# Optimization experiments

Hardware: AMD Instinct MI355X
Metric: run time of the kernel (lower is better)

## Reference

```python
import jax, jax.numpy as jnp
import numpy as np

B, T1, T2, F, H = 4, 1024, 2048, 1024, 16
DK = F // H


def setup_inputs() -> dict:
    key = jax.random.key(0)
    ks = jax.random.split(key, 9)
    s = 1.0 / np.sqrt(F)
    return {
        "x": jax.random.normal(ks[0], (B, T1, F), dtype=jnp.float32),
        "memory": jax.random.normal(ks[1], (B, T2, F), dtype=jnp.float32),
        "memory_mask": jax.random.randint(ks[2], (B, 1, T2), 0, 2, dtype=jnp.int32),
        "Wq": jax.random.normal(ks[3], (F, F), dtype=jnp.float32) * s,
        "bq": jnp.zeros((F,), dtype=jnp.float32),
        "Wkv": jax.random.normal(ks[4], (F, 2 * F), dtype=jnp.float32) * s,
        "bkv": jnp.zeros((2 * F,), dtype=jnp.float32),
        "Wo": jax.random.normal(ks[5], (F, F), dtype=jnp.float32) * s,
        "bo": jnp.zeros((F,), dtype=jnp.float32),
    }


def reference(x, memory, memory_mask, Wq, bq, Wkv, bkv, Wo, bo):
    b = x.shape[0]
    # QKV projections
    q = (x @ Wq + bq).reshape(b, -1, H, DK).transpose(0, 2, 1, 3)      # [b,h,t1,dk]
    kv = memory @ Wkv + bkv
    k, v = jnp.split(kv, 2, axis=-1)
    k = k.reshape(b, -1, H, DK).transpose(0, 2, 1, 3)                   # [b,h,t2,dk]
    v = v.reshape(b, -1, H, DK).transpose(0, 2, 1, 3)                   # [b,h,t2,dk]
    # scaled dot-product scores [b,h,t1,t2]
    scores = jnp.einsum("bhqd,bhkd->bhqk", q * (DK ** -0.5), k)
    # mask (b,1,t2) -> (b,1,1,t2); eq(0) means masked out
    m = (memory_mask[:, None, :, :] == 0)
    scores = jnp.where(m, -jnp.inf, scores)
    attn = jax.nn.softmax(scores, axis=-1)
    attn = jnp.where(m, 0.0, attn)
    out = jnp.einsum("bhqk,bhkd->bhqd", attn, v)                        # [b,h,t1,dk]
    out = out.transpose(0, 2, 1, 3).reshape(b, -1, H * DK)              # [b,t1,F]
    return out @ Wo + bo
```

## Files before the change

kernel.cpp:

```cpp
#include <hip/hip_runtime.h>

typedef unsigned short u16;
typedef __attribute__((ext_vector_type(8))) short bf16x8;
typedef __attribute__((ext_vector_type(4))) float f32x4;
typedef __attribute__((ext_vector_type(4))) unsigned u32x4;

#define DEVI __device__ __forceinline__

static constexpr int B_ = 4, T1 = 1024, T2 = 2048, F = 1024, H = 16, DK = 64;

typedef __attribute__((address_space(3))) unsigned lds_u32;
typedef __attribute__((address_space(1))) const unsigned gmem_u32;

DEVI u16 f2bf(float f) {
    union { float f; unsigned u; } c; c.f = f;
    unsigned u = c.u + 0x7fffu + ((c.u >> 16) & 1u);
    return (u16)(u >> 16);
}

__global__ __launch_bounds__(256) void cast2_bf16_k(const float* __restrict__ a, u16* __restrict__ da, int na,
                                                    const float* __restrict__ b, u16* __restrict__ db, int ntot) {
    int i = (blockIdx.x * 256 + threadIdx.x) * 4;
    if (i >= ntot) return;
    const float* s = (i < na) ? a : b;
    u16* d = (i < na) ? da : db;
    int off = (i < na) ? i : i - na;
    float4 v = *(const float4*)(s + off);
    ushort4 o;
    o.x = f2bf(v.x); o.y = f2bf(v.y); o.z = f2bf(v.z); o.w = f2bf(v.w);
    *(ushort4*)(d + off) = o;
}

__global__ __launch_bounds__(256) void transpose_cast_k(const float* __restrict__ src0,
                                                        u16* __restrict__ dst0,
                                                        const float* __restrict__ src1,
                                                        u16* __restrict__ dst1,
                                                        int K, int N) {
    const float* src = blockIdx.z ? src1 : src0;
    u16* dst = blockIdx.z ? dst1 : dst0;
    __shared__ float tile[64][65];
    int kb = blockIdx.x * 64, nb = blockIdx.y * 64;
    int tx = threadIdx.x & 63, ty = threadIdx.x >> 6;
#pragma unroll
    for (int p = 0; p < 16; ++p) {
        int r = p * 4 + ty;
        tile[r][tx] = src[(size_t)(kb + r) * N + nb + tx];
    }
    __syncthreads();
#pragma unroll
    for (int p = 0; p < 16; ++p) {
        int r = p * 4 + ty;
        dst[(size_t)(nb + r) * K + kb + tx] = f2bf(tile[tx][r]);
    }
}

template <bool OUT_BF16, int WM, int WN>
__global__ __launch_bounds__(256) void gemm_k(const u16* __restrict__ A,
                                              const u16* __restrict__ Bt,
                                              const float* __restrict__ bias,
                                              float scale,
                                              void* __restrict__ Cout,
                                              int M, int N, int K) {
    constexpr int BM = 2 * WM, BN = 2 * WN;
    __shared__ u16 ldsA[2][BM * 64];
    __shared__ u16 ldsB[2][BN * 64];
    const int t = threadIdx.x;
    const int w = t >> 6, lane = t & 63;
    const int wr = w >> 1, wc = w & 1;
    const int lr = lane & 15, lg = lane >> 4;

    const int r0 = t >> 3;
    const int cl = (t & 7) ^ (r0 & 7);
    const u16* Ag = A + (size_t)(blockIdx.x * BM + r0) * K + cl * 8;
    const u16* Bg = Bt + (size_t)(blockIdx.y * BN + r0) * K + cl * 8;

#define GSTAGE(BUF, KOFF) \
    { \
        _Pragma("unroll") \
        for (int i_ = 0; i_ < BM / 32; ++i_) \
            __builtin_amdgcn_global_load_lds( \
                (gmem_u32*)(Ag + (size_t)i_ * 32 * K + (KOFF)), \
                (lds_u32*)((char*)&ldsA[BUF][0] + i_ * 4096 + w * 1024), 16, 0, 0); \
        _Pragma("unroll") \
        for (int i_ = 0; i_ < BN / 32; ++i_) \
            __builtin_amdgcn_global_load_lds( \
                (gmem_u32*)(Bg + (size_t)i_ * 32 * K + (KOFF)), \
                (lds_u32*)((char*)&ldsB[BUF][0] + i_ * 4096 + w * 1024), 16, 0, 0); \
    }

    f32x4 acc[WM / 16][WN / 16] = {};

    GSTAGE(0, 0);
    __syncthreads();

    int buf = 0;
    for (int k0 = 0; k0 < K; k0 += 64) {
        if (k0 + 64 < K) GSTAGE(buf ^ 1, k0 + 64);

        bf16x8 a[2][WM / 16], b[2][WN / 16];
#pragma unroll
        for (int kk = 0; kk < 2; ++kk) {
#pragma unroll
            for (int m = 0; m < WM / 16; ++m) {
                int ra = wr * WM + m * 16 + lr;
                a[kk][m] = *(const bf16x8*)&ldsA[buf][ra * 64 + (((kk * 4 + lg) ^ (ra & 7)) * 8)];
            }
#pragma unroll
            for (int n = 0; n < WN / 16; ++n) {
                int rb = wc * WN + n * 16 + lr;
                b[kk][n] = *(const bf16x8*)&ldsB[buf][rb * 64 + (((kk * 4 + lg) ^ (rb & 7)) * 8)];
            }
        }
#pragma unroll
        for (int kk = 0; kk < 2; ++kk)
#pragma unroll
            for (int m = 0; m < WM / 16; ++m)
#pragma unroll
                for (int n = 0; n < WN / 16; ++n)
                    acc[m][n] = __builtin_amdgcn_mfma_f32_16x16x32_bf16(a[kk][m], b[kk][n], acc[m][n], 0, 0, 0);
        __syncthreads();
        buf ^= 1;
    }

    const int rbase = blockIdx.x * BM + wr * WM;
    const int cbase = blockIdx.y * BN + wc * WN;
#pragma unroll
    for (int m = 0; m < WM / 16; ++m)
#pragma unroll
        for (int n = 0; n < WN / 16; ++n) {
            int col = cbase + n * 16 + lr;
            float bv = bias ? bias[col] : 0.f;
#pragma unroll
            for (int j = 0; j < 4; ++j) {
                int row = rbase + m * 16 + lg * 4 + j;
                float v = (acc[m][n][j] + bv) * scale;
                if (OUT_BF16)
                    ((u16*)Cout)[(size_t)row * N + col] = f2bf(v);
                else
                    ((float*)Cout)[(size_t)row * N + col] = v;
            }
        }
#undef GSTAGE
}

__global__ __launch_bounds__(256) void gemm_kv_k(const u16* __restrict__ A,
                                                 const u16* __restrict__ Bt,
                                                 const float* __restrict__ bias,
                                                 u16* __restrict__ Kb,
                                                 u16* __restrict__ Vt) {
    constexpr int K = F, N = F;
    __shared__ u16 smem[4][128 * 64];
    const int t = threadIdx.x;
    const int w = t >> 6, lane = t & 63;
    const int wr = w >> 1, wc = w & 1;
    const int lr = lane & 15, lg = lane >> 4;

    const int r0 = t >> 3;
    const int cl = (t & 7) ^ (r0 & 7);
    const u16* Ag = A + (size_t)(blockIdx.x * 128 + r0) * K + cl * 8;
    const u16* Bg = Bt + (size_t)(blockIdx.y * 128 + r0) * K + cl * 8;

#define KVSTAGE(BUF, KOFF) \
    { \
        _Pragma("unroll") \
        for (int i_ = 0; i_ < 4; ++i_) { \
            __builtin_amdgcn_global_load_lds( \
                (gmem_u32*)(Ag + (size_t)i_ * 32 * K + (KOFF)), \
                (lds_u32*)((char*)&smem[BUF][0] + i_ * 4096 + w * 1024), 16, 0, 0); \
            __builtin_amdgcn_global_load_lds( \
                (gmem_u32*)(Bg + (size_t)i_ * 32 * K + (KOFF)), \
                (lds_u32*)((char*)&smem[2 + (BUF)][0] + i_ * 4096 + w * 1024), 16, 0, 0); \
        } \
    }

    f32x4 acc[4][4] = {};

    KVSTAGE(0, 0);
    __syncthreads();

    int buf = 0;
    for (int k0 = 0; k0 < K; k0 += 64) {
        if (k0 + 64 < K) KVSTAGE(buf ^ 1, k0 + 64);

        bf16x8 a[2][4], b[2][4];
#pragma unroll
        for (int kk = 0; kk < 2; ++kk)
#pragma unroll
            for (int m = 0; m < 4; ++m) {
                int ra = wr * 64 + m * 16 + lr;
                int rb = wc * 64 + m * 16 + lr;
                a[kk][m] = *(const bf16x8*)&smem[buf][ra * 64 + (((kk * 4 + lg) ^ (ra & 7)) * 8)];
                b[kk][m] = *(const bf16x8*)&smem[2 + buf][rb * 64 + (((kk * 4 + lg) ^ (rb & 7)) * 8)];
            }
#pragma unroll
        for (int kk = 0; kk < 2; ++kk)
#pragma unroll
            for (int m = 0; m < 4; ++m)
#pragma unroll
                for (int n = 0; n < 4; ++n)
                    acc[m][n] = __builtin_amdgcn_mfma_f32_16x16x32_bf16(a[kk][m], b[kk][n], acc[m][n], 0, 0, 0);
        __syncthreads();
        buf ^= 1;
    }

    const int rbase = blockIdx.x * 128 + wr * 64;
    if (blockIdx.y < 8) {
        const int cbase = blockIdx.y * 128 + wc * 64;
#pragma unroll
        for (int m = 0; m < 4; ++m)
#pragma unroll
            for (int n = 0; n < 4; ++n) {
                int col = cbase + n * 16 + lr;
                float bv = bias[col];
#pragma unroll
                for (int j = 0; j < 4; ++j) {
                    int row = rbase + m * 16 + lg * 4 + j;
                    Kb[(size_t)row * N + col] = f2bf(acc[m][n][j] + bv);
                }
            }
    } else {
        u16* tbuf = &smem[0][0];
        const int cb2 = (blockIdx.y - 8) * 128;
#pragma unroll
        for (int m = 0; m < 4; ++m)
#pragma unroll
            for (int n = 0; n < 4; ++n) {
                int c = wc * 64 + n * 16 + lr;
                float bv = bias[F + cb2 + c];
#pragma unroll
                for (int j = 0; j < 4; ++j) {
                    int r = wr * 64 + m * 16 + lg * 4 + j;
                    int np = ((r >> 2) & 3) * 16 + ((r >> 5) & 1) * 8 + ((r >> 4) & 1) * 4 + (r & 3) + (r & 64);
                    tbuf[c * 136 + np] = f2bf(acc[m][n][j] + bv);
                }
            }
        __syncthreads();
        const int c = t >> 1, half = t & 1;
        const int rb = blockIdx.x * 128;
        const int b = rb >> 11, t2b = rb & 2047;
        const int vcol = cb2 + c;
        const int hh = vcol >> 6, d = vcol & 63;
        u16* dst = Vt + ((size_t)((b * H + hh) * DK + d)) * T2 + t2b + half * 64;
        const u16* srcp = &tbuf[c * 136 + half * 64];
#pragma unroll
        for (int i = 0; i < 8; ++i)
            *(uint4*)(dst + i * 8) = *(const uint4*)(srcp + i * 8);
    }
#undef KVSTAGE
}

#define SOFTMAX_PACK(S, PA0, PA1) \
    { \
        float pv_[4][4]; \
        _Pragma("unroll") \
        for (int ss_ = 0; ss_ < 4; ++ss_) \
            _Pragma("unroll") \
            for (int j_ = 0; j_ < 4; ++j_) \
                pv_[ss_][j_] = __builtin_amdgcn_exp2f(S[ss_][j_]); \
        u32x4 pw0_, pw1_; \
        asm("v_cvt_pk_bf16_f32 %0, %1, %2" : "=v"(pw0_[0]) : "v"(pv_[0][0]), "v"(pv_[0][1])); \
        asm("v_cvt_pk_bf16_f32 %0, %1, %2" : "=v"(pw0_[1]) : "v"(pv_[0][2]), "v"(pv_[0][3])); \
        asm("v_cvt_pk_bf16_f32 %0, %1, %2" : "=v"(pw0_[2]) : "v"(pv_[1][0]), "v"(pv_[1][1])); \
        asm("v_cvt_pk_bf16_f32 %0, %1, %2" : "=v"(pw0_[3]) : "v"(pv_[1][2]), "v"(pv_[1][3])); \
        asm("v_cvt_pk_bf16_f32 %0, %1, %2" : "=v"(pw1_[0]) : "v"(pv_[2][0]), "v"(pv_[2][1])); \
        asm("v_cvt_pk_bf16_f32 %0, %1, %2" : "=v"(pw1_[1]) : "v"(pv_[2][2]), "v"(pv_[2][3])); \
        asm("v_cvt_pk_bf16_f32 %0, %1, %2" : "=v"(pw1_[2]) : "v"(pv_[3][0]), "v"(pv_[3][1])); \
        asm("v_cvt_pk_bf16_f32 %0, %1, %2" : "=v"(pw1_[3]) : "v"(pv_[3][2]), "v"(pv_[3][3])); \
        PA0 = __builtin_bit_cast(bf16x8, pw0_); \
        PA1 = __builtin_bit_cast(bf16x8, pw1_); \
    }

__global__ __launch_bounds__(256) void attn_k(const u16* __restrict__ Qb,
                                              const u16* __restrict__ Kb,
                                              const u16* __restrict__ Vt,
                                              const int* __restrict__ mask,
                                              u16* __restrict__ attO) {
    __shared__ u16 ldsK[2][64 * 64];
    __shared__ u16 ldsV[2][64 * 64];
    __shared__ float smaskf[T2];

    const int h = blockIdx.x, q0 = blockIdx.y * 128, b = blockIdx.z;
    const int w = threadIdx.x >> 6, lane = threadIdx.x & 63;
    const int lr = lane & 15, lg = lane >> 4;

    for (int i = threadIdx.x; i < T2; i += 256)
        smaskf[i] = mask[b * T2 + i] ? -16.f : -1e30f;

    const u16* qptrA = Qb + (size_t)(b * T1 + q0 + w * 32 + lr) * F + h * DK + lg * 8;
    const bf16x8 qA0 = *(const bf16x8*)(qptrA);
    const bf16x8 qA1 = *(const bf16x8*)(qptrA + 32);
    const bf16x8 qB0 = *(const bf16x8*)(qptrA + 16 * F);
    const bf16x8 qB1 = *(const bf16x8*)(qptrA + 16 * F + 32);

    u32x4 ow; ow[0] = ow[1] = ow[2] = ow[3] = 0x3F803F80u;
    const bf16x8 onesf = __builtin_bit_cast(bf16x8, ow);

    const u16* Kg = Kb + (size_t)b * T2 * F + h * DK;
    const u16* Vg = Vt + (size_t)(b * H + h) * DK * T2;
    const int sr = (lane >> 3);
    const int scd = lane & 7;

#define STAGE(BUF, KT) \
    { \
        if (w < 2) { \
            _Pragma("unroll") \
            for (int i_ = 0; i_ < 4; ++i_) { \
                int ii_ = (w & 1) * 4 + i_; \
                int r0_ = ii_ * 8 + sr; \
                int cl_ = scd ^ (r0_ & 7); \
                __builtin_amdgcn_global_load_lds( \
                    (gmem_u32*)(Kg + (size_t)((KT) * 64 + r0_) * F + cl_ * 8), \
                    (lds_u32*)((char*)&ldsK[BUF][0] + ii_ * 1024), 16, 0, 0); \
            } \
        } else { \
            _Pragma("unroll") \
            for (int i_ = 0; i_ < 4; ++i_) { \
                int ii_ = (w & 1) * 4 + i_; \
                int r0_ = ii_ * 8 + sr; \
                int cl_ = scd ^ (r0_ & 7); \
                __builtin_amdgcn_global_load_lds( \
                    (gmem_u32*)(Vg + (size_t)r0_ * T2 + (KT) * 64 + cl_ * 8), \
                    (lds_u32*)((char*)&ldsV[BUF][0] + ii_ * 1024), 16, 0, 0); \
            } \
        } \
    }

    f32x4 oA[4] = {}, oB[4] = {};
    f32x4 lsA4 = {}, lsB4 = {};

    STAGE(0, 0);
    __syncthreads();

    int buf = 0;
    for (int kt = 0; kt < T2 / 64; ++kt) {
        if (kt < T2 / 64 - 1) STAGE(buf ^ 1, kt + 1);

        bf16x8 kf[4][2], vf[2][4];
#pragma unroll
        for (int ss = 0; ss < 4; ++ss) {
            int row = ss * 16 + lr;
            kf[ss][0] = *(const bf16x8*)&ldsK[buf][row * 64 + ((lg ^ (row & 7)) * 8)];
            kf[ss][1] = *(const bf16x8*)&ldsK[buf][row * 64 + (((4 + lg) ^ (row & 7)) * 8)];
        }
#pragma unroll
        for (int m = 0; m < 2; ++m)
#pragma unroll
            for (int d = 0; d < 4; ++d) {
                int row = d * 16 + lr;
                vf[m][d] = *(const bf16x8*)&ldsV[buf][row * 64 + (((lg * 2 + m) ^ (row & 7)) * 8)];
            }

        f32x4 sA[4], sB[4];
#pragma unroll
        for (int ss = 0; ss < 4; ++ss) {
            f32x4 c = *(const f32x4*)&smaskf[kt * 64 + ss * 16 + lg * 4];
            sA[ss] = c; sB[ss] = c;
        }
        __builtin_amdgcn_s_setprio(1);
#pragma unroll
        for (int ss = 0; ss < 4; ++ss) {
            sA[ss] = __builtin_amdgcn_mfma_f32_16x16x32_bf16(kf[ss][0], qA0, sA[ss], 0, 0, 0);
            sB[ss] = __builtin_amdgcn_mfma_f32_16x16x32_bf16(kf[ss][0], qB0, sB[ss], 0, 0, 0);
            sA[ss] = __builtin_amdgcn_mfma_f32_16x16x32_bf16(kf[ss][1], qA1, sA[ss], 0, 0, 0);
            sB[ss] = __builtin_amdgcn_mfma_f32_16x16x32_bf16(kf[ss][1], qB1, sB[ss], 0, 0, 0);
        }
        __builtin_amdgcn_s_setprio(0);

        bf16x8 paA0, paA1, paB0, paB1;
        SOFTMAX_PACK(sA, paA0, paA1);
        SOFTMAX_PACK(sB, paB0, paB1);

        __builtin_amdgcn_s_setprio(1);
#pragma unroll
        for (int d = 0; d < 4; ++d) {
            oA[d] = __builtin_amdgcn_mfma_f32_16x16x32_bf16(vf[0][d], paA0, oA[d], 0, 0, 0);
            oB[d] = __builtin_amdgcn_mfma_f32_16x16x32_bf16(vf[0][d], paB0, oB[d], 0, 0, 0);
        }
        lsA4 = __builtin_amdgcn_mfma_f32_16x16x32_bf16(onesf, paA0, lsA4, 0, 0, 0);
        lsB4 = __builtin_amdgcn_mfma_f32_16x16x32_bf16(onesf, paB0, lsB4, 0, 0, 0);
#pragma unroll
        for (int d = 0; d < 4; ++d) {
            oA[d] = __builtin_amdgcn_mfma_f32_16x16x32_bf16(vf[1][d], paA1, oA[d], 0, 0, 0);
            oB[d] = __builtin_amdgcn_mfma_f32_16x16x32_bf16(vf[1][d], paB1, oB[d], 0, 0, 0);
        }
        lsA4 = __builtin_amdgcn_mfma_f32_16x16x32_bf16(onesf, paA1, lsA4, 0, 0, 0);
        lsB4 = __builtin_amdgcn_mfma_f32_16x16x32_bf16(onesf, paB1, lsB4, 0, 0, 0);
        __builtin_amdgcn_s_setprio(0);

        __syncthreads();
        buf ^= 1;
    }

    float invA = lsA4[0] > 0.f ? 1.f / lsA4[0] : 1.f;
    float invB = lsB4[0] > 0.f ? 1.f / lsB4[0] : 1.f;
    const size_t obase = (size_t)(b * T1 + q0 + w * 32 + lr) * F + h * DK;
#pragma unroll
    for (int d = 0; d < 4; ++d) {
        ushort4 oa, ob;
        oa.x = f2bf(oA[d][0] * invA); oa.y = f2bf(oA[d][1] * invA);
        oa.z = f2bf(oA[d][2] * invA); oa.w = f2bf(oA[d][3] * invA);
        ob.x = f2bf(oB[d][0] * invB); ob.y = f2bf(oB[d][1] * invB);
        ob.z = f2bf(oB[d][2] * invB); ob.w = f2bf(oB[d][3] * invB);
        *(ushort4*)&attO[obase + d * 16 + lg * 4] = oa;
        *(ushort4*)&attO[obase + 16 * F + d * 16 + lg * 4] = ob;
    }
}

extern "C" void kernel_launch(void* const* d_in, const int* in_sizes, int n_in,
                              void* d_out, int out_size, void* d_ws, size_t ws_size,
                              hipStream_t stream) {
    const float* x      = (const float*)d_in[0];
    const float* memory = (const float*)d_in[1];
    const int*   mmask  = (const int*)d_in[2];
    const float* Wq     = (const float*)d_in[3];
    const float* bq     = (const float*)d_in[4];
    const float* Wkv    = (const float*)d_in[5];
    const float* bkv    = (const float*)d_in[6];
    const float* Wo     = (const float*)d_in[7];
    const float* bo     = (const float*)d_in[8];
    float* out = (float*)d_out;
    char* ws = (char*)d_ws;

    u16* xb   = (u16*)(ws);
    u16* mb   = (u16*)(ws + (8u  << 20));
    u16* Wqt  = (u16*)(ws + (24u << 20));
    u16* Wkvt = (u16*)(ws + (26u << 20));
    u16* Wot  = (u16*)(ws + (30u << 20));
    u16* Qb   = (u16*)(ws + (32u << 20));
    u16* Kb   = (u16*)(ws + (40u << 20));
    u16* Vt   = (u16*)(ws + (56u << 20));
    u16* attO = xb;

    cast2_bf16_k<<<(B_ * T1 * F + B_ * T2 * F) / 1024, 256, 0, stream>>>(
        x, xb, B_ * T1 * F, memory, mb, B_ * T1 * F + B_ * T2 * F);

    transpose_cast_k<<<dim3(F / 64, F / 64, 2), 256, 0, stream>>>(Wq, Wqt, Wo, Wot, F, F);
    transpose_cast_k<<<dim3(F / 64, 2 * F / 64, 1), 256, 0, stream>>>(Wkv, Wkvt, Wkv, Wkvt, F, 2 * F);

    gemm_k<true, 32, 64><<<dim3(B_ * T1 / 64, F / 128), 256, 0, stream>>>(xb, Wqt, bq, 0.125f * 1.44269504f, Qb, B_ * T1, F, F);
    gemm_kv_k<<<dim3(B_ * T2 / 128, 2 * F / 128), 256, 0, stream>>>(mb, Wkvt, bkv, Kb, Vt);

    attn_k<<<dim3(H, T1 / 128, B_), 256, 0, stream>>>(Qb, Kb, Vt, mmask, attO);

    gemm_k<false, 32, 64><<<dim3(B_ * T1 / 64, F / 128), 256, 0, stream>>>(attO, Wot, bo, 1.f, out, B_ * T1, F, F);
}
```

Measured before the change: 142.7 us.

## Split attention key range across two wave groups per block with LDS reduction

The attention kernel now launches 512 threads per block. Two groups of four waves each process alternating 64-key tiles, each with its own double-buffered K/V LDS staging. At the end, group 1 writes its partial output accumulators and row sums into LDS, and group 0 adds them before normalizing and storing. This doubles in-flight waves per block to hide latency in the serial key loop, at the cost of twice the LDS footprint, an extra reduction pass, and possibly lower block occupancy per CU.

```diff
diff --git a/kernel.cpp b/kernel.cpp
--- a/kernel.cpp
+++ b/kernel.cpp
@@ -270,23 +270,24 @@
         PA1 = __builtin_bit_cast(bf16x8, pw1_); \
     }
 
-__global__ __launch_bounds__(256) void attn_k(const u16* __restrict__ Qb,
+__global__ __launch_bounds__(512) void attn_k(const u16* __restrict__ Qb,
                                               const u16* __restrict__ Kb,
                                               const u16* __restrict__ Vt,
                                               const int* __restrict__ mask,
                                               u16* __restrict__ attO) {
-    __shared__ u16 ldsK[2][64 * 64];
-    __shared__ u16 ldsV[2][64 * 64];
+    __shared__ u16 ldsK[2][2][64 * 64];
+    __shared__ u16 ldsV[2][2][64 * 64];
     __shared__ float smaskf[T2];
 
     const int h = blockIdx.x, q0 = blockIdx.y * 128, b = blockIdx.z;
     const int w = threadIdx.x >> 6, lane = threadIdx.x & 63;
+    const int g = w >> 2, wg = w & 3;
     const int lr = lane & 15, lg = lane >> 4;
 
-    for (int i = threadIdx.x; i < T2; i += 256)
+    for (int i = threadIdx.x; i < T2; i += 512)
         smaskf[i] = mask[b * T2 + i] ? -16.f : -1e30f;
 
-    const u16* qptrA = Qb + (size_t)(b * T1 + q0 + w * 32 + lr) * F + h * DK + lg * 8;
+    const u16* qptrA = Qb + (size_t)(b * T1 + q0 + wg * 32 + lr) * F + h * DK + lg * 8;
     const bf16x8 qA0 = *(const bf16x8*)(qptrA);
     const bf16x8 qA1 = *(const bf16x8*)(qptrA + 32);
     const bf16x8 qB0 = *(const bf16x8*)(qptrA + 16 * F);
@@ -295,32 +296,32 @@
     u32x4 ow; ow[0] = ow[1] = ow[2] = ow[3] = 0x3F803F80u;
     const bf16x8 onesf = __builtin_bit_cast(bf16x8, ow);
 
-    const u16* Kg = Kb + (size_t)b * T2 * F + h * DK;
-    const u16* Vg = Vt + (size_t)(b * H + h) * DK * T2;
+    const u16* Kg_ = Kb + (size_t)b * T2 * F + h * DK;
+    const u16* Vg_ = Vt + (size_t)(b * H + h) * DK * T2;
     const int sr = (lane >> 3);
     const int scd = lane & 7;
 
-#define STAGE(BUF, KT) \
+#define STAGE(PB, KT) \
     { \
-        if (w < 2) { \
+        if (wg < 2) { \
             _Pragma("unroll") \
             for (int i_ = 0; i_ < 4; ++i_) { \
-                int ii_ = (w & 1) * 4 + i_; \
+                int ii_ = (wg & 1) * 4 + i_; \
                 int r0_ = ii_ * 8 + sr; \
                 int cl_ = scd ^ (r0_ & 7); \
                 __builtin_amdgcn_global_load_lds( \
-                    (gmem_u32*)(Kg + (size_t)((KT) * 64 + r0_) * F + cl_ * 8), \
-                    (lds_u32*)((char*)&ldsK[BUF][0] + ii_ * 1024), 16, 0, 0); \
+                    (gmem_u32*)(Kg_ + (size_t)((KT) * 64 + r0_) * F + cl_ * 8), \
+                    (lds_u32*)((char*)&ldsK[g][PB][0] + ii_ * 1024), 16, 0, 0); \
             } \
         } else { \
             _Pragma("unroll") \
             for (int i_ = 0; i_ < 4; ++i_) { \
-                int ii_ = (w & 1) * 4 + i_; \
+                int ii_ = (wg & 1) * 4 + i_; \
                 int r0_ = ii_ * 8 + sr; \
                 int cl_ = scd ^ (r0_ & 7); \
                 __builtin_amdgcn_global_load_lds( \
-                    (gmem_u32*)(Vg + (size_t)r0_ * T2 + (KT) * 64 + cl_ * 8), \
-                    (lds_u32*)((char*)&ldsV[BUF][0] + ii_ * 1024), 16, 0, 0); \
+                    (gmem_u32*)(Vg_ + (size_t)r0_ * T2 + (KT) * 64 + cl_ * 8), \
+                    (lds_u32*)((char*)&ldsV[g][PB][0] + ii_ * 1024), 16, 0, 0); \
             } \
         } \
     }
@@ -328,26 +329,27 @@
     f32x4 oA[4] = {}, oB[4] = {};
     f32x4 lsA4 = {}, lsB4 = {};
 
-    STAGE(0, 0);
+    STAGE(0, g);
     __syncthreads();
 
     int buf = 0;
-    for (int kt = 0; kt < T2 / 64; ++kt) {
-        if (kt < T2 / 64 - 1) STAGE(buf ^ 1, kt + 1);
+    for (int i = 0; i < 16; ++i) {
+        const int kt = 2 * i + g;
+        if (i < 15) STAGE(buf ^ 1, kt + 2);
 
         bf16x8 kf[4][2], vf[2][4];
 #pragma unroll
         for (int ss = 0; ss < 4; ++ss) {
             int row = ss * 16 + lr;
-            kf[ss][0] = *(const bf16x8*)&ldsK[buf][row * 64 + ((lg ^ (row & 7)) * 8)];
-            kf[ss][1] = *(const bf16x8*)&ldsK[buf][row * 64 + (((4 + lg) ^ (row & 7)) * 8)];
+            kf[ss][0] = *(const bf16x8*)&ldsK[g][buf][row * 64 + ((lg ^ (row & 7)) * 8)];
+            kf[ss][1] = *(const bf16x8*)&ldsK[g][buf][row * 64 + (((4 + lg) ^ (row & 7)) * 8)];
         }
 #pragma unroll
         for (int m = 0; m < 2; ++m)
 #pragma unroll
             for (int d = 0; d < 4; ++d) {
                 int row = d * 16 + lr;
-                vf[m][d] = *(const bf16x8*)&ldsV[buf][row * 64 + (((lg * 2 + m) ^ (row & 7)) * 8)];
+                vf[m][d] = *(const bf16x8*)&ldsV[g][buf][row * 64 + (((lg * 2 + m) ^ (row & 7)) * 8)];
             }
 
         f32x4 sA[4], sB[4];
@@ -391,18 +393,43 @@
         buf ^= 1;
     }
 
-    float invA = lsA4[0] > 0.f ? 1.f / lsA4[0] : 1.f;
-    float invB = lsB4[0] > 0.f ? 1.f / lsB4[0] : 1.f;
-    const size_t obase = (size_t)(b * T1 + q0 + w * 32 + lr) * F + h * DK;
-#pragma unroll
-    for (int d = 0; d < 4; ++d) {
-        ushort4 oa, ob;
-        oa.x = f2bf(oA[d][0] * invA); oa.y = f2bf(oA[d][1] * invA);
-        oa.z = f2bf(oA[d][2] * invA); oa.w = f2bf(oA[d][3] * invA);
-        ob.x = f2bf(oB[d][0] * invB); ob.y = f2bf(oB[d][1] * invB);
-        ob.z = f2bf(oB[d][2] * invB); ob.w = f2bf(oB[d][3] * invB);
-        *(ushort4*)&attO[obase + d * 16 + lg * 4] = oa;
-        *(ushort4*)&attO[obase + 16 * F + d * 16 + lg * 4] = ob;
+    float* cO = (float*)&ldsK[0][0][0];
+    float* cL = (float*)&ldsV[0][0][0];
+    const int cb = (wg * 64 + lane) * 32;
+    const int sw = (lane & 7) << 2;
+    if (g == 1) {
+#pragma unroll
+        for (int c = 0; c < 4; ++c)
+            *(f32x4*)&cO[cb + ((c * 4) ^ sw)] = oA[c];
+#pragma unroll
+        for (int c = 0; c < 4; ++c)
+            *(f32x4*)&cO[cb + (((c + 4) * 4) ^ sw)] = oB[c];
+        cL[(wg * 64 + lane) * 2] = lsA4[0];
+        cL[(wg * 64 + lane) * 2 + 1] = lsB4[0];
+    }
+    __syncthreads();
+    if (g == 0) {
+#pragma unroll
+        for (int c = 0; c < 4; ++c)
+            oA[c] += *(const f32x4*)&cO[cb + ((c * 4) ^ sw)];
+#pragma unroll
+        for (int c = 0; c < 4; ++c)
+            oB[c] += *(const f32x4*)&cO[cb + (((c + 4) * 4) ^ sw)];
+        float lA = lsA4[0] + cL[(wg * 64 + lane) * 2];
+        float lB = lsB4[0] + cL[(wg * 64 + lane) * 2 + 1];
+        float invA = lA > 0.f ? 1.f / lA : 1.f;
+        float invB = lB > 0.f ? 1.f / lB : 1.f;
+        const size_t obase = (size_t)(b * T1 + q0 + wg * 32 + lr) * F + h * DK;
+#pragma unroll
+        for (int d = 0; d < 4; ++d) {
+            ushort4 oa, ob;
+            oa.x = f2bf(oA[d][0] * invA); oa.y = f2bf(oA[d][1] * invA);
+            oa.z = f2bf(oA[d][2] * invA); oa.w = f2bf(oA[d][3] * invA);
+            ob.x = f2bf(oB[d][0] * invB); ob.y = f2bf(oB[d][1] * invB);
+            ob.z = f2bf(oB[d][2] * invB); ob.w = f2bf(oB[d][3] * invB);
+            *(ushort4*)&attO[obase + d * 16 + lg * 4] = oa;
+            *(ushort4*)&attO[obase + 16 * F + d * 16 + lg * 4] = ob;
+        }
     }
 }
 
@@ -440,7 +467,7 @@
     gemm_k<true, 32, 64><<<dim3(B_ * T1 / 64, F / 128), 256, 0, stream>>>(xb, Wqt, bq, 0.125f * 1.44269504f, Qb, B_ * T1, F, F);
     gemm_kv_k<<<dim3(B_ * T2 / 128, 2 * F / 128), 256, 0, stream>>>(mb, Wkvt, bkv, Kb, Vt);
 
-    attn_k<<<dim3(H, T1 / 128, B_), 256, 0, stream>>>(Qb, Kb, Vt, mmask, attO);
+    attn_k<<<dim3(H, T1 / 128, B_), 512, 0, stream>>>(Qb, Kb, Vt, mmask, attO);
 
     gemm_k<false, 32, 64><<<dim3(B_ * T1 / 64, F / 128), 256, 0, stream>>>(attO, Wot, bo, 1.f, out, B_ * T1, F, F);
 }
```

Result: slower. 153.2 us (+7.4%).
